# Kernel optimization log

Hardware: AMD Instinct MI355X
Metric: run time of the kernel (lower is better)

Reference implementation:

```python
import jax, jax.numpy as jnp
import numpy as np
from jax import lax

BATCH, SEQ, NMEAS, HID, STATIC, TEMB = 8, 2048, 37, 256, 8, 32
NL, DIN, NST, RANK, K, NLAB = 4, 512, 16, 16, 4, 2  # DIN=expand*HID, RANK=ceil(HID/16)


def rmsnorm(x, w, eps=1e-5):
    return x * lax.rsqrt(jnp.mean(x * x, -1, keepdims=True) + eps) * w


def causal_depthwise_conv(x, w, b):
    # x: [B,L,D], w: [D,K], b: [D]
    L = x.shape[1]
    xpad = jnp.pad(x, ((0, 0), (K - 1, 0), (0, 0)))
    y = sum(w[:, k] * xpad[:, k:k + L, :] for k in range(K))
    return y + b


def selective_scan(u, dt, Bm, Cm, A, Dv):
    # u, dt: [B,L,D]; Bm, Cm: [B,L,N]; A: [D,N]; Dv: [D]
    def step(h, inp):
        dt_t, B_t, C_t, u_t = inp  # [B,D],[B,N],[B,N],[B,D]
        dA = jnp.exp(dt_t[..., None] * A)                      # [B,D,N]
        h = dA * h + dt_t[..., None] * B_t[:, None, :] * u_t[..., None]
        y = jnp.einsum('bdn,bn->bd', h, C_t)
        return h, y

    h0 = jnp.zeros((u.shape[0], DIN, NST), u.dtype)
    xs = (dt.transpose(1, 0, 2), Bm.transpose(1, 0, 2), Cm.transpose(1, 0, 2), u.transpose(1, 0, 2))
    _, ys = lax.scan(step, h0, xs)
    return ys.transpose(1, 0, 2) + u * Dv


def mamba_block(h, nw, ipW, cW, cb, xpW, dpW, dpb, Alog, Dv, opW):
    x = rmsnorm(h, nw)
    proj = x @ ipW.T                     # [B,L,2*DIN]
    xi, z = proj[..., :DIN], proj[..., DIN:]
    xc = jax.nn.silu(causal_depthwise_conv(xi, cW, cb))
    xdbc = xc @ xpW.T                    # [B,L,RANK+2N]
    dt = jax.nn.softplus(xdbc[..., :RANK] @ dpW.T + dpb)
    Bm = xdbc[..., RANK:RANK + NST]
    Cm = xdbc[..., RANK + NST:]
    A = -jnp.exp(Alog)
    y = selective_scan(xc, dt, Bm, Cm, A, Dv)
    y = y * jax.nn.silu(z)
    return h + y @ opW.T


def _forward(time_series_data, static_data, time_array, ts_W, ts_b, t2v_w, t2v_b,
             time_W, time_b, static_W, static_b, ln_g, ln_b, norm_w, in_proj_W,
             conv_W, conv_b, x_proj_W, dt_proj_W, dt_proj_b, A_log, D_skip,
             out_proj_W, normf_w, dense_W, dense_b, head_W, head_b):
    # embeddings: measurement projection + time2vec + static broadcast, then LayerNorm
    x = jnp.einsum('bmt,hm->bth', time_series_data, ts_W) + ts_b    # [B,T,H]
    tv = time_array[..., None] * t2v_w + t2v_b                       # [B,T,TEMB]
    tv = jnp.concatenate([tv[..., :1], jnp.sin(tv[..., 1:])], -1)    # time2vec
    x = x + tv @ time_W.T + time_b
    x = x + (static_data @ static_W.T + static_b)[:, None, :]
    mu = jnp.mean(x, -1, keepdims=True)
    var = jnp.var(x, -1, keepdims=True)
    h = (x - mu) * lax.rsqrt(var + 1e-12) * ln_g + ln_b
    for i in range(NL):
        h = mamba_block(h, norm_w[i], in_proj_W[i], conv_W[i], conv_b[i],
                        x_proj_W[i], dt_proj_W[i], dt_proj_b[i], A_log[i],
                        D_skip[i], out_proj_W[i])
    h = rmsnorm(h, normf_w)
    pooled = jnp.mean(h, 1)                                          # [B,H]
    z = jax.nn.relu(pooled @ dense_W.T + dense_b)
    return z @ head_W.T + head_b                                     # [B,NLAB]


def setup_inputs() -> dict:
    key = jax.random.key(0)
    ks = iter(jax.random.split(key, 48))
    rn = lambda *s: jax.random.normal(next(ks), s, jnp.float32)
    sc = 0.02
    d = {}
    d['time_series_data'] = rn(BATCH, NMEAS, SEQ)
    d['static_data'] = rn(BATCH, STATIC)
    d['time_array'] = jax.random.uniform(next(ks), (BATCH, SEQ), jnp.float32) * 100.0
    d['ts_W'] = rn(HID, NMEAS) * sc; d['ts_b'] = jnp.zeros(HID)
    d['t2v_w'] = rn(TEMB) * sc; d['t2v_b'] = rn(TEMB) * sc
    d['time_W'] = rn(HID, TEMB) * sc; d['time_b'] = jnp.zeros(HID)
    d['static_W'] = rn(HID, STATIC) * sc; d['static_b'] = jnp.zeros(HID)
    d['ln_g'] = jnp.ones(HID); d['ln_b'] = jnp.zeros(HID)
    d['norm_w'] = jnp.ones((NL, HID))
    d['in_proj_W'] = rn(NL, 2 * DIN, HID) * sc
    d['conv_W'] = rn(NL, DIN, K) * sc; d['conv_b'] = jnp.zeros((NL, DIN))
    d['x_proj_W'] = rn(NL, RANK + 2 * NST, DIN) * sc
    d['dt_proj_W'] = rn(NL, DIN, RANK) * sc
    d['dt_proj_b'] = jnp.full((NL, DIN), -4.6) + rn(NL, DIN) * 0.1
    d['A_log'] = jnp.tile(jnp.log(jnp.arange(1, NST + 1, dtype=jnp.float32)), (NL, DIN, 1))
    d['D_skip'] = jnp.ones((NL, DIN))
    d['out_proj_W'] = rn(NL, HID, DIN) * sc
    d['normf_w'] = jnp.ones(HID)
    d['dense_W'] = rn(HID, HID) * sc; d['dense_b'] = jnp.zeros(HID)
    d['head_W'] = rn(NLAB, HID) * sc; d['head_b'] = jnp.zeros(NLAB)
    return d


def reference(time_series_data, static_data, time_array, ts_W, ts_b, t2v_w, t2v_b,
              time_W, time_b, static_W, static_b, ln_g, ln_b, norm_w, in_proj_W,
              conv_W, conv_b, x_proj_W, dt_proj_W, dt_proj_b, A_log, D_skip,
              out_proj_W, normf_w, dense_W, dense_b, head_W, head_b):
    return _forward(time_series_data, static_data, time_array, ts_W, ts_b, t2v_w,
                    t2v_b, time_W, time_b, static_W, static_b, ln_g, ln_b, norm_w,
                    in_proj_W, conv_W, conv_b, x_proj_W, dt_proj_W, dt_proj_b,
                    A_log, D_skip, out_proj_W, normf_w, dense_W, dense_b, head_W, head_b)
```

## Files before the change

### kernel.cpp

```cpp
#include <hip/hip_runtime.h>
#include <math.h>

#define B_ 8
#define T_ 2048
#define HID_ 256
#define DIN_ 512
#define NST_ 16
#define RANK_ 16
#define NL_ 4
#define NC_ 128
#define TC_ 16

typedef unsigned short u16;
typedef unsigned int u32;
typedef __attribute__((ext_vector_type(8))) short bf16x8;
typedef __attribute__((ext_vector_type(4))) float f32x4;

__device__ __forceinline__ float exp2_i(float x) {
  float r; asm("v_exp_f32 %0, %1" : "=v"(r) : "v"(x)); return r;
}
__device__ __forceinline__ float log2_i(float x) {
  float r; asm("v_log_f32 %0, %1" : "=v"(r) : "v"(x)); return r;
}
__device__ __forceinline__ float rcp_i(float x) {
  float r; asm("v_rcp_f32 %0, %1" : "=v"(r) : "v"(x)); return r;
}
#define LOG2E 1.44269504f
#define LN2   0.69314718f

__device__ __forceinline__ float silu_f(float x) {
  return x * rcp_i(1.f + exp2_i(-LOG2E * x));
}
__device__ __forceinline__ float softplus_f(float x) {
  return (x > 20.f) ? x : LN2 * log2_i(1.f + exp2_i(LOG2E * x));
}

__device__ __forceinline__ u16 f2b(float f) {
  union { float f; unsigned u; } v; v.f = f;
  unsigned r = (v.u + 0x7FFFu + ((v.u >> 16) & 1u)) >> 16;
  return (u16)r;
}
__device__ __forceinline__ float b2f(u16 b) {
  union { unsigned u; float f; } v; v.u = ((unsigned)b) << 16;
  return v.f;
}

__device__ __forceinline__ void async16(const void* g, const void* l) {
  __builtin_amdgcn_global_load_lds(
      (const __attribute__((address_space(1))) unsigned int*)g,
      (__attribute__((address_space(3))) unsigned int*)l, 16, 0, 0);
}

__global__ __launch_bounds__(256) void f2b_k(const float* __restrict__ s, u16* __restrict__ d, int n)
{
  int i = (blockIdx.x * 256 + threadIdx.x) * 4;
  if (i + 3 < n) {
    float4 v = *(const float4*)(s + i);
    d[i + 0] = f2b(v.x); d[i + 1] = f2b(v.y); d[i + 2] = f2b(v.z); d[i + 3] = f2b(v.w);
  } else {
    for (int k = i; k < n; k++) d[k] = f2b(s[k]);
  }
}

__global__ __launch_bounds__(256) void a2t_k(const float* __restrict__ Alog, float* __restrict__ a2t)
{
  int idx = blockIdx.x * 256 + threadIdx.x;
  int l = idx >> 13, nd = idx & 8191;
  int n = nd >> 9, d = nd & 511;
  float al = Alog[(size_t)l * 8192 + d * 16 + n];
  a2t[(size_t)l * 8192 + n * 512 + d] = -exp2_i(al * LOG2E) * LOG2E;
}

__global__ __launch_bounds__(512) void wmerge_k(
    const float* __restrict__ dpW,
    const float* __restrict__ xpW,
    u16* __restrict__ wcomb)
{
  int n = blockIdx.x, l = blockIdx.y, k = threadIdx.x;
  const float* xp = xpW + (size_t)l * 48 * 512;
  float acc;
  if (n < 512) {
    const float* dp = dpW + ((size_t)l * 512 + n) * 16;
    acc = 0.f;
    #pragma unroll
    for (int r = 0; r < 16; r++) acc += dp[r] * xp[r * 512 + k];
  } else if (n < 544) {
    acc = xp[(size_t)(16 + n - 512) * 512 + k];
  } else {
    acc = 0.f;
  }
  wcomb[((size_t)l * 640 + n) * 512 + k] = f2b(acc);
}

__global__ __launch_bounds__(256) void embed_ln_k(
    const float* __restrict__ tsd, const float* __restrict__ stat, const float* __restrict__ ta,
    const float* __restrict__ tsW, const float* __restrict__ tsb,
    const float* __restrict__ t2vw, const float* __restrict__ t2vb,
    const float* __restrict__ timeW, const float* __restrict__ timeb,
    const float* __restrict__ statW, const float* __restrict__ statb,
    const float* __restrict__ lng, const float* __restrict__ lnb,
    const float* __restrict__ nw0,
    float* __restrict__ hout, u16* __restrict__ xnb)
{
  __shared__ float xts[37 * 32];
  __shared__ float tvs[32 * 32];
  __shared__ float outs[32 * 257];
  __shared__ float smu[32], srs[32], srs2[32];
  int blk = blockIdx.x;
  int b = blk >> 6, t0 = (blk & 63) * 32;
  int j = threadIdx.x;

  float wts[37], wtv[32], wst[8];
  #pragma unroll
  for (int m = 0; m < 37; m++) wts[m] = tsW[j * 37 + m];
  #pragma unroll
  for (int e = 0; e < 32; e++) wtv[e] = timeW[j * 32 + e];
  #pragma unroll
  for (int s = 0; s < 8; s++) wst[s] = statW[j * 8 + s];
  float biasj = tsb[j] + timeb[j] + statb[j];
  float lngj = lng[j], lnbj = lnb[j];
  float nw0j = nw0[j];
  float stq[8];
  #pragma unroll
  for (int s = 0; s < 8; s++) stq[s] = stat[b * 8 + s];

  for (int idx = j; idx < 37 * 32; idx += 256) {
    int m = idx >> 5, tt = idx & 31;
    xts[idx] = tsd[((size_t)b * 37 + m) * T_ + t0 + tt];
  }
  {
    int rr = j >> 5, ee = j & 31;
    #pragma unroll
    for (int rp = 0; rp < 4; rp++) {
      int r = rp * 8 + rr;
      float tav = ta[b * T_ + t0 + r];
      float tv = tav * t2vw[ee] + t2vb[ee];
      tvs[r * 32 + ee] = (ee == 0) ? tv : sinf(tv);
    }
  }
  __syncthreads();

  for (int r = 0; r < 32; r++) {
    float acc = biasj;
    #pragma unroll
    for (int m = 0; m < 37; m++) acc += xts[m * 32 + r] * wts[m];
    #pragma unroll
    for (int e = 0; e < 32; e++) acc += tvs[r * 32 + e] * wtv[e];
    #pragma unroll
    for (int s = 0; s < 8; s++) acc += stq[s] * wst[s];
    outs[r * 257 + j] = acc;
  }
  __syncthreads();
  {
    int r = j >> 3, q = j & 7;
    const float* po = &outs[r * 257 + q * 32];
    float s = 0.f, ss = 0.f;
    #pragma unroll
    for (int i = 0; i < 32; i++) { float v = po[i]; s += v; ss += v * v; }
    s += __shfl_down(s, 1, 64); ss += __shfl_down(ss, 1, 64);
    s += __shfl_down(s, 2, 64); ss += __shfl_down(ss, 2, 64);
    s += __shfl_down(s, 4, 64); ss += __shfl_down(ss, 4, 64);
    if (q == 0) {
      float mu = s * (1.f / 256.f);
      smu[r] = mu;
      srs[r] = rsqrtf(ss * (1.f / 256.f) - mu * mu + 1e-12f);
    }
  }
  __syncthreads();
  for (int r = 0; r < 32; r++) {
    float v = outs[r * 257 + j];
    float hv = (v - smu[r]) * srs[r] * lngj + lnbj;
    hout[((size_t)(b * T_ + t0 + r)) * HID_ + j] = hv;
    outs[r * 257 + j] = hv;
  }
  __syncthreads();
  {
    int r = j >> 3, q = j & 7;
    const float* po = &outs[r * 257 + q * 32];
    float ss = 0.f;
    #pragma unroll
    for (int i = 0; i < 32; i++) { float v = po[i]; ss += v * v; }
    ss += __shfl_down(ss, 1, 64);
    ss += __shfl_down(ss, 2, 64);
    ss += __shfl_down(ss, 4, 64);
    if (q == 0) srs2[r] = rsqrtf(ss * (1.f / 256.f) + 1e-5f);
  }
  __syncthreads();
  for (int r = 0; r < 32; r++) {
    xnb[((size_t)(b * T_ + t0 + r)) * HID_ + j] = f2b(outs[r * 257 + j] * srs2[r] * nw0j);
  }
}

template <int MODE>
__global__ __launch_bounds__(256) void mgemm_k(
    const u16* __restrict__ A, int lda,
    const u16* __restrict__ W, int ldw,
    void* __restrict__ Cv, int ldc,
    int K,
    const float* __restrict__ bias,
    void* __restrict__ Cv2)
{
  __shared__ u16 smem[128 * 136];
  u16* sA = smem;
  u16* sB = smem + 128 * 64;
  const int tid = threadIdx.x;
  const int bm = blockIdx.x * 128, bn = blockIdx.y * 128;
  const int w = tid >> 6, l = tid & 63;
  const int wm = (w & 1) * 64, wn = (w >> 1) * 64;
  const int lr = l & 15, lh = l >> 4;

  f32x4 acc[4][4] = {};

  const int srow = tid >> 3;
  const int schunk = tid & 7;

  for (int k0 = 0; k0 < K; k0 += 64) {
    #pragma unroll
    for (int c = 0; c < 4; c++) {
      int row = c * 32 + srow;
      int g = schunk ^ (row & 7);
      async16(A + (size_t)(bm + row) * lda + k0 + g * 8, &sA[c * 2048 + w * 512]);
      async16(W + (size_t)(bn + row) * ldw + k0 + g * 8, &sB[c * 2048 + w * 512]);
    }
    __syncthreads();
    #pragma unroll
    for (int kk = 0; kk < 2; kk++) {
      bf16x8 af[4], bfr[4];
      #pragma unroll
      for (int i = 0; i < 4; i++) {
        int ra = wm + i * 16 + lr;
        int rb = wn + i * 16 + lr;
        int e = kk * 4 + lh;
        af[i]  = *(const bf16x8*)&sA[ra * 64 + ((e ^ (ra & 7)) * 8)];
        bfr[i] = *(const bf16x8*)&sB[rb * 64 + ((e ^ (rb & 7)) * 8)];
      }
      #pragma unroll
      for (int i = 0; i < 4; i++)
        #pragma unroll
        for (int j = 0; j < 4; j++)
          acc[i][j] = __builtin_amdgcn_mfma_f32_16x16x32_bf16(af[i], bfr[j], acc[i][j], 0, 0, 0);
    }
    __syncthreads();
  }

  if (MODE == 6 && bn >= 512) {
    #pragma unroll
    for (int i = 0; i < 4; i++) {
      int m = bm + wm + i * 16 + lh * 4;
      #pragma unroll
      for (int j = 0; j < 4; j++) {
        int n = bn + wn + j * 16 + lr;
        if (n < 544) {
          #pragma unroll
          for (int r = 0; r < 4; r++)
            ((float*)Cv2)[(size_t)(m + r) * 32 + (n - 512)] = acc[i][j][r];
        }
      }
    }
  } else {
    u16* eps = smem;
    float bv[4];
    if (MODE == 6) {
      #pragma unroll
      for (int j = 0; j < 4; j++) bv[j] = bias[bn + wn + j * 16 + lr];
    }
    #pragma unroll
    for (int i = 0; i < 4; i++) {
      int rr = wm + i * 16 + lh * 4;
      #pragma unroll
      for (int j = 0; j < 4; j++) {
        int cc = wn + j * 16 + lr;
        #pragma unroll
        for (int r = 0; r < 4; r++) {
          float v = acc[i][j][r];
          if (MODE == 6) v = softplus_f(v + bv[j]);
          eps[(rr + r) * 136 + cc] = f2b(v);
        }
      }
    }
    __syncthreads();
    u16* dbase; int c0;
    if (MODE == 4 && bn >= 512) { dbase = (u16*)Cv2; c0 = bn - 512; }
    else                        { dbase = (u16*)Cv;  c0 = bn; }
    #pragma unroll
    for (int q = 0; q < 8; q++) {
      int flat = q * 256 + tid;
      int row = flat >> 4, cv = flat & 15;
      *(uint4*)&dbase[(size_t)(bm + row) * 512 + c0 + cv * 8] =
          *(const uint4*)&eps[row * 136 + cv * 8];
    }
  }
}

__global__ __launch_bounds__(256) void mgemm7_k(
    const u16* __restrict__ A,
    const u16* __restrict__ W,
    float* __restrict__ h,
    const float* __restrict__ nw,
    u16* __restrict__ xnb)
{
  __shared__ u16 smem[20480];
  __shared__ float rns[2][64];
  __shared__ float snw[256];
  u16* sA = smem;
  u16* sB = smem + 4096;
  const int tid = threadIdx.x;
  const int bm = blockIdx.x * 64;
  const int w = tid >> 6, l = tid & 63;
  const int wm = (w & 1) * 32, wn = (w >> 1) * 128;
  const int lr = l & 15, lh = l >> 4;

  if (tid < 256) snw[tid] = nw[tid];

  f32x4 acc[2][8] = {};

  const int srow = tid >> 3;
  const int schunk = tid & 7;

  for (int k0 = 0; k0 < 512; k0 += 64) {
    #pragma unroll
    for (int c = 0; c < 2; c++) {
      int row = c * 32 + srow;
      int g = schunk ^ (row & 7);
      async16(A + (size_t)(bm + row) * 512 + k0 + g * 8, &sA[c * 2048 + w * 512]);
    }
    #pragma unroll
    for (int c = 0; c < 8; c++) {
      int row = c * 32 + srow;
      int g = schunk ^ (row & 7);
      async16(W + (size_t)row * 512 + k0 + g * 8, &sB[c * 2048 + w * 512]);
    }
    __syncthreads();
    #pragma unroll
    for (int kk = 0; kk < 2; kk++) {
      int e = kk * 4 + lh;
      bf16x8 af[2], bfr[8];
      #pragma unroll
      for (int i = 0; i < 2; i++) {
        int ra = wm + i * 16 + lr;
        af[i] = *(const bf16x8*)&sA[ra * 64 + ((e ^ (ra & 7)) * 8)];
      }
      #pragma unroll
      for (int j = 0; j < 8; j++) {
        int rb = wn + j * 16 + lr;
        bfr[j] = *(const bf16x8*)&sB[rb * 64 + ((e ^ (rb & 7)) * 8)];
      }
      #pragma unroll
      for (int i = 0; i < 2; i++)
        #pragma unroll
        for (int j = 0; j < 8; j++)
          acc[i][j] = __builtin_amdgcn_mfma_f32_16x16x32_bf16(af[i], bfr[j], acc[i][j], 0, 0, 0);
    }
    __syncthreads();
  }

  #pragma unroll
  for (int i = 0; i < 2; i++) {
    int m = bm + wm + i * 16 + lh * 4;
    #pragma unroll
    for (int j = 0; j < 8; j++) {
      int n = wn + j * 16 + lr;
      float* cp = h + (size_t)m * 256 + n;
      #pragma unroll
      for (int r = 0; r < 4; r++) {
        float hv = acc[i][j][r] + cp[(size_t)r * 256];
        cp[(size_t)r * 256] = hv;
        acc[i][j][r] = hv;
      }
    }
  }
  #pragma unroll
  for (int i = 0; i < 2; i++) {
    #pragma unroll
    for (int r = 0; r < 4; r++) {
      float p = 0.f;
      #pragma unroll
      for (int j = 0; j < 8; j++) { float v = acc[i][j][r]; p += v * v; }
      p += __shfl_xor(p, 1, 64);
      p += __shfl_xor(p, 2, 64);
      p += __shfl_xor(p, 4, 64);
      p += __shfl_xor(p, 8, 64);
      if (lr == 0) rns[w >> 1][wm + i * 16 + lh * 4 + r] = p;
    }
  }
  __syncthreads();
  u16* eps = smem;
  #pragma unroll
  for (int i = 0; i < 2; i++) {
    #pragma unroll
    for (int r = 0; r < 4; r++) {
      int rl = wm + i * 16 + lh * 4 + r;
      float rs = rsqrtf((rns[0][rl] + rns[1][rl]) * (1.f / 256.f) + 1e-5f);
      #pragma unroll
      for (int j = 0; j < 8; j++) {
        int n = wn + j * 16 + lr;
        eps[rl * 264 + n] = f2b(acc[i][j][r] * rs * snw[n]);
      }
    }
  }
  __syncthreads();
  #pragma unroll
  for (int q = 0; q < 8; q++) {
    int flat = q * 256 + tid;
    int row = flat >> 5, cv = flat & 31;
    *(uint4*)&xnb[(size_t)(bm + row) * 256 + cv * 8] =
        *(const uint4*)&eps[row * 264 + cv * 8];
  }
}

__global__ __launch_bounds__(256) void conv_silu_k(
    const u16* __restrict__ xib,
    const float* __restrict__ cw,
    const float* __restrict__ cb,
    u16* __restrict__ xcb)
{
  int idx = blockIdx.x * 256 + threadIdx.x;
  int row = idx >> 6;
  int t = row & (T_ - 1);
  int d0 = (idx & 63) << 3;

  float acc[8];
  *(float4*)&acc[0] = *(const float4*)&cb[d0];
  *(float4*)&acc[4] = *(const float4*)&cb[d0 + 4];
  float wreg[8][4];
  #pragma unroll
  for (int j = 0; j < 8; j++)
    *(float4*)&wreg[j][0] = *(const float4*)&cw[(d0 + j) * 4];

  #pragma unroll
  for (int k = 0; k < 4; k++) {
    int tt = t + k - 3;
    if (tt >= 0) {
      bf16x8 v = *(const bf16x8*)&xib[(size_t)(row + k - 3) * 512 + d0];
      #pragma unroll
      for (int j = 0; j < 8; j++) acc[j] += wreg[j][k] * b2f((u16)v[j]);
    }
  }
  u16 o[8];
  #pragma unroll
  for (int j = 0; j < 8; j++) o[j] = f2b(silu_f(acc[j]));
  *(bf16x8*)&xcb[(size_t)row * 512 + d0] = *(const bf16x8*)o;
}

__global__ __launch_bounds__(512) void scan_passA_k(
    const u16* __restrict__ xcb,
    const u16* __restrict__ dtb,
    const float* __restrict__ xdbc,
    const float* __restrict__ a2t,
    u16* __restrict__ chH, float* __restrict__ dts)
{
  __shared__ float sDBC[TC_ * 32];
  int c = blockIdx.x, b = blockIdx.y, d = threadIdx.x;
  size_t base_row = (size_t)(b * T_ + c * TC_);

  if (d < 128) async16(xdbc + base_row * 32 + d * 4, &sDBC[(d >> 6) * 256]);

  float a2[16], hl[16];
  #pragma unroll
  for (int n = 0; n < 16; n++) { a2[n] = a2t[n * 512 + d]; hl[n] = 0.f; }
  float dtsum = 0.f;
  const u16* up = xcb + base_row * 512 + d;
  const u16* tp = dtb + base_row * 512 + d;
  u16 pu = up[0], pt = tp[0];
  __syncthreads();

  #pragma unroll 1
  for (int s = 0; s < TC_; s++) {
    float u   = b2f(pu);
    float dtv = b2f(pt);
    int sn = (s + 1 < TC_) ? s + 1 : s;
    pu = up[(size_t)sn * 512];
    pt = tp[(size_t)sn * 512];
    dtsum += dtv;
    float du = dtv * u;
    const float* rowp = &sDBC[s * 32];
    #pragma unroll
    for (int g = 0; g < 4; g++) {
      float4 b4 = *(const float4*)&rowp[g * 4];
      int i = g * 4;
      float dA0 = exp2_i(dtv * a2[i + 0]); hl[i + 0] = dA0 * hl[i + 0] + du * b4.x;
      float dA1 = exp2_i(dtv * a2[i + 1]); hl[i + 1] = dA1 * hl[i + 1] + du * b4.y;
      float dA2 = exp2_i(dtv * a2[i + 2]); hl[i + 2] = dA2 * hl[i + 2] + du * b4.z;
      float dA3 = exp2_i(dtv * a2[i + 3]); hl[i + 3] = dA3 * hl[i + 3] + du * b4.w;
    }
  }
  u16 oh[16];
  #pragma unroll
  for (int n = 0; n < 16; n++) oh[n] = f2b(hl[n]);
  size_t o = ((size_t)((b * NC_ + c) * DIN_ + d)) * 16;
  *(uint4*)&chH[o]     = *(const uint4*)&oh[0];
  *(uint4*)&chH[o + 8] = *(const uint4*)&oh[8];
  dts[(size_t)(b * NC_ + c) * DIN_ + d] = dtsum;
}

__global__ __launch_bounds__(256) void scan_mid_k(
    const u32* __restrict__ chH32, const float* __restrict__ dts,
    const float* __restrict__ a2t, u32* __restrict__ hin32)
{
  int idx = blockIdx.x * 256 + threadIdx.x;
  int b = idx >> 12, dk = idx & 4095;
  int d = dk >> 3, k = dk & 7;
  float a20 = a2t[(2 * k) * 512 + d];
  float a21 = a2t[(2 * k + 1) * 512 + d];
  float h0 = 0.f, h1 = 0.f;
  #pragma unroll 8
  for (int c = 0; c < NC_; c++) {
    size_t o = ((size_t)(b * NC_ + c)) * 4096 + dk;
    u32 hh = chH32[o];
    float dsv = dts[(size_t)(b * NC_ + c) * 512 + d];
    hin32[o] = ((u32)f2b(h1) << 16) | (u32)f2b(h0);
    float ap0 = exp2_i(a20 * dsv);
    float ap1 = exp2_i(a21 * dsv);
    h0 = ap0 * h0 + b2f((u16)(hh & 0xffff));
    h1 = ap1 * h1 + b2f((u16)(hh >> 16));
  }
}

__global__ __launch_bounds__(512) void scan_passC_k(
    const u16* __restrict__ xcb,
    const u16* __restrict__ dtb,
    const u16* __restrict__ zb,
    const float* __restrict__ xdbc,
    const float* __restrict__ a2t,
    const u16* __restrict__ hin,
    const float* __restrict__ Dv,
    u16* __restrict__ yzb)
{
  __shared__ float sDBC[TC_ * 32];
  int c = blockIdx.x, b = blockIdx.y, d = threadIdx.x;
  size_t base_row = (size_t)(b * T_ + c * TC_);

  if (d < 128) async16(xdbc + base_row * 32 + d * 4, &sDBC[(d >> 6) * 256]);

  float a2[16], hs[16];
  {
    size_t ho = ((size_t)((b * NC_ + c) * DIN_ + d)) * 16;
    uint4 h0 = *(const uint4*)&hin[ho];
    uint4 h1 = *(const uint4*)&hin[ho + 8];
    const u32* hw = (const u32*)&h0;
    #pragma unroll
    for (int j = 0; j < 4; j++) {
      hs[2 * j]     = b2f((u16)(hw[j] & 0xffff));
      hs[2 * j + 1] = b2f((u16)(hw[j] >> 16));
    }
    const u32* hw1 = (const u32*)&h1;
    #pragma unroll
    for (int j = 0; j < 4; j++) {
      hs[8 + 2 * j]     = b2f((u16)(hw1[j] & 0xffff));
      hs[8 + 2 * j + 1] = b2f((u16)(hw1[j] >> 16));
    }
  }
  #pragma unroll
  for (int n = 0; n < 16; n++) a2[n] = a2t[n * 512 + d];
  float dv = Dv[d];
  const u16* up = xcb + base_row * 512 + d;
  const u16* tp = dtb + base_row * 512 + d;
  const u16* zp = zb + base_row * 512 + d;
  u16 pu = up[0], pt = tp[0], zz = zp[0];
  __syncthreads();

  #pragma unroll 1
  for (int s = 0; s < TC_; s++) {
    float u   = b2f(pu);
    float dtv = b2f(pt);
    float z   = b2f(zz);
    int sn = (s + 1 < TC_) ? s + 1 : s;
    pu = up[(size_t)sn * 512];
    pt = tp[(size_t)sn * 512];
    zz = zp[(size_t)sn * 512];
    float du = dtv * u;
    float y = 0.f;
    const float* rowp = &sDBC[s * 32];
    #pragma unroll
    for (int g = 0; g < 4; g++) {
      float4 b4 = *(const float4*)&rowp[g * 4];
      float4 c4 = *(const float4*)&rowp[16 + g * 4];
      int i = g * 4;
      float dA0 = exp2_i(dtv * a2[i + 0]); hs[i + 0] = dA0 * hs[i + 0] + du * b4.x; y += hs[i + 0] * c4.x;
      float dA1 = exp2_i(dtv * a2[i + 1]); hs[i + 1] = dA1 * hs[i + 1] + du * b4.y; y += hs[i + 1] * c4.y;
      float dA2 = exp2_i(dtv * a2[i + 2]); hs[i + 2] = dA2 * hs[i + 2] + du * b4.z; y += hs[i + 2] * c4.z;
      float dA3 = exp2_i(dtv * a2[i + 3]); hs[i + 3] = dA3 * hs[i + 3] + du * b4.w; y += hs[i + 3] * c4.w;
    }
    y += u * dv;
    yzb[(base_row + s) * DIN_ + d] = f2b(y * silu_f(z));
  }
}

__global__ __launch_bounds__(256) void pool_partial_k(const u16* __restrict__ xn, float* __restrict__ poolP)
{
  int b = blockIdx.x, tc = blockIdx.y, j = threadIdx.x;
  float s = 0.f;
  int t0 = tc * 256;
  #pragma unroll 4
  for (int tt = 0; tt < 256; tt++)
    s += b2f(xn[((size_t)(b * T_ + t0 + tt)) * HID_ + j]);
  poolP[(b * 8 + tc) * HID_ + j] = s;
}

__global__ __launch_bounds__(256) void head_k(
    const float* __restrict__ poolP,
    const float* __restrict__ denW, const float* __restrict__ denb,
    const float* __restrict__ hdW, const float* __restrict__ hdb,
    float* __restrict__ out)
{
  int b = blockIdx.x, j = threadIdx.x;
  float p = 0.f;
  #pragma unroll
  for (int tc = 0; tc < 8; tc++) p += poolP[(b * 8 + tc) * HID_ + j];
  p *= (1.f / 2048.f);
  __shared__ float pl[256], zs[256];
  pl[j] = p;
  __syncthreads();
  float acc = denb[j];
  #pragma unroll 8
  for (int k = 0; k < 256; k++) acc += pl[k] * denW[j * 256 + k];
  zs[j] = fmaxf(acc, 0.f);
  __syncthreads();
  if (j < 2) {
    float o = hdb[j];
    for (int k = 0; k < 256; k++) o += zs[k] * hdW[j * 256 + k];
    out[b * 2 + j] = o;
  }
}

extern "C" void kernel_launch(void* const* d_in, const int* in_sizes, int n_in,
                              void* d_out, int out_size, void* d_ws, size_t ws_size,
                              hipStream_t stream)
{
  const float* tsd   = (const float*)d_in[0];
  const float* stat  = (const float*)d_in[1];
  const float* ta    = (const float*)d_in[2];
  const float* tsW   = (const float*)d_in[3];
  const float* tsb   = (const float*)d_in[4];
  const float* t2vw  = (const float*)d_in[5];
  const float* t2vb  = (const float*)d_in[6];
  const float* timeW = (const float*)d_in[7];
  const float* timeb = (const float*)d_in[8];
  const float* statW = (const float*)d_in[9];
  const float* statb = (const float*)d_in[10];
  const float* lng   = (const float*)d_in[11];
  const float* lnb   = (const float*)d_in[12];
  const float* normw = (const float*)d_in[13];
  const float* ipW   = (const float*)d_in[14];
  const float* convW = (const float*)d_in[15];
  const float* convb = (const float*)d_in[16];
  const float* xpW   = (const float*)d_in[17];
  const float* dpW   = (const float*)d_in[18];
  const float* dpb   = (const float*)d_in[19];
  const float* Alog  = (const float*)d_in[20];
  const float* Dsk   = (const float*)d_in[21];
  const float* opW   = (const float*)d_in[22];
  const float* normf = (const float*)d_in[23];
  const float* denW  = (const float*)d_in[24];
  const float* denb  = (const float*)d_in[25];
  const float* hdW   = (const float*)d_in[26];
  const float* hdb   = (const float*)d_in[27];
  float* out = (float*)d_out;

  float* ws = (float*)d_ws;
  float* h    = ws;  ws += (size_t)B_ * T_ * HID_;
  float* xdbc = ws;  ws += (size_t)B_ * T_ * 32;
  float* poolP= ws;  ws += (size_t)B_ * 8 * HID_;
  float* a2t  = ws;  ws += (size_t)NL_ * NST_ * DIN_;
  float* dts  = ws;  ws += (size_t)B_ * NC_ * DIN_;
  u16* chH    = (u16*)ws;  ws += (size_t)B_ * NC_ * DIN_ * NST_ / 2;
  u16* hin    = (u16*)ws;  ws += (size_t)B_ * NC_ * DIN_ * NST_ / 2;
  u16* dtb    = (u16*)ws;  ws += (size_t)B_ * T_ * DIN_ / 2;
  u16* xi_b   = (u16*)ws;  ws += (size_t)B_ * T_ * DIN_ / 2;
  u16* z_b    = (u16*)ws;  ws += (size_t)B_ * T_ * DIN_ / 2;
  u16* xn_b   = (u16*)ws;  ws += (size_t)B_ * T_ * HID_ / 2;
  u16* xcb    = (u16*)ws;  ws += (size_t)B_ * T_ * DIN_ / 2;
  u16* yz_b   = (u16*)ws;  ws += (size_t)B_ * T_ * DIN_ / 2;
  u16* wipb   = (u16*)ws;  ws += (size_t)NL_ * 1024 * HID_ / 2;
  u16* wopb   = (u16*)ws;  ws += (size_t)NL_ * HID_ * DIN_ / 2;
  u16* wcomb  = (u16*)ws;  ws += (size_t)NL_ * 640 * DIN_ / 2;

  const int ROWS = B_ * T_;

  {
    int nip = NL_ * 1024 * HID_;
    int nop = NL_ * HID_ * DIN_;
    f2b_k<<<nip / 1024, 256, 0, stream>>>(ipW, wipb, nip);
    f2b_k<<<nop / 1024, 256, 0, stream>>>(opW, wopb, nop);
    a2t_k<<<NL_ * NST_ * DIN_ / 256, 256, 0, stream>>>(Alog, a2t);
    wmerge_k<<<dim3(640, NL_), 512, 0, stream>>>(dpW, xpW, wcomb);
  }

  embed_ln_k<<<512, 256, 0, stream>>>(tsd, stat, ta, tsW, tsb, t2vw, t2vb,
                                      timeW, timeb, statW, statb, lng, lnb,
                                      normw, h, xn_b);

  for (int i = 0; i < NL_; i++) {
    const u16* wipbi = wipb + (size_t)i * 1024 * HID_;
    const u16* wopbi = wopb + (size_t)i * HID_ * DIN_;
    const u16* wcombi = wcomb + (size_t)i * 640 * DIN_;
    const float* dpbi = dpb + (size_t)i * DIN_;
    const float* a2ti = a2t + (size_t)i * NST_ * DIN_;
    const float* nw_next = (i < NL_ - 1) ? (normw + (i + 1) * HID_) : normf;

    mgemm_k<4><<<dim3(ROWS / 128, 8), 256, 0, stream>>>(
        xn_b, HID_, wipbi, HID_, xi_b, 512, HID_, nullptr, z_b);
    conv_silu_k<<<ROWS * 64 / 256, 256, 0, stream>>>(xi_b, convW + i * DIN_ * 4, convb + i * DIN_, xcb);
    mgemm_k<6><<<dim3(ROWS / 128, 5), 256, 0, stream>>>(
        xcb, DIN_, wcombi, DIN_, dtb, 512, DIN_, dpbi, xdbc);
    scan_passA_k<<<dim3(NC_, B_), DIN_, 0, stream>>>(xcb, dtb, xdbc, a2ti, chH, dts);
    scan_mid_k<<<B_ * DIN_ * 8 / 256, 256, 0, stream>>>((const u32*)chH, dts, a2ti, (u32*)hin);
    scan_passC_k<<<dim3(NC_, B_), DIN_, 0, stream>>>(xcb, dtb, z_b, xdbc, a2ti, hin,
                                                     Dsk + i * DIN_, yz_b);
    mgemm7_k<<<ROWS / 64, 256, 0, stream>>>(yz_b, wopbi, h, nw_next, xn_b);
  }

  pool_partial_k<<<dim3(B_, 8), 256, 0, stream>>>(xn_b, poolP);
  head_k<<<B_, 256, 0, stream>>>(poolP, denW, denb, hdW, hdb, out);
}
```

Before: 700.4 us.

## Fuse pooling into final out-proj GEMM, merge prep kernels, register-reuse conv

On the last layer, the output-projection GEMM now reduces the normalized rows straight into per-batch pooled sums with atomics, so it no longer writes h, the bf16 xn buffer or runs a separate pooling kernel. The weight-conversion and A-transform kernels are merged into one launch. The causal conv now computes four timesteps per thread, reusing the loaded input rows from registers. Atomic accumulation changes the floating-point summation order, and a memset is added.

```diff
diff --git a/kernel.cpp b/kernel.cpp
--- a/kernel.cpp
+++ b/kernel.cpp
@@ -51,24 +51,29 @@
       (__attribute__((address_space(3))) unsigned int*)l, 16, 0, 0);
 }
 
-__global__ __launch_bounds__(256) void f2b_k(const float* __restrict__ s, u16* __restrict__ d, int n)
-{
-  int i = (blockIdx.x * 256 + threadIdx.x) * 4;
-  if (i + 3 < n) {
-    float4 v = *(const float4*)(s + i);
-    d[i + 0] = f2b(v.x); d[i + 1] = f2b(v.y); d[i + 2] = f2b(v.z); d[i + 3] = f2b(v.w);
+__global__ __launch_bounds__(256) void prep_k(
+    const float* __restrict__ ipW, u16* __restrict__ wipb,
+    const float* __restrict__ opW, u16* __restrict__ wopb,
+    const float* __restrict__ Alog, float* __restrict__ a2t)
+{
+  int blk = blockIdx.x;
+  if (blk < 1024) {
+    int i = (blk * 256 + threadIdx.x) * 4;
+    float4 v = *(const float4*)(ipW + i);
+    wipb[i + 0] = f2b(v.x); wipb[i + 1] = f2b(v.y);
+    wipb[i + 2] = f2b(v.z); wipb[i + 3] = f2b(v.w);
+  } else if (blk < 1536) {
+    int i = ((blk - 1024) * 256 + threadIdx.x) * 4;
+    float4 v = *(const float4*)(opW + i);
+    wopb[i + 0] = f2b(v.x); wopb[i + 1] = f2b(v.y);
+    wopb[i + 2] = f2b(v.z); wopb[i + 3] = f2b(v.w);
   } else {
-    for (int k = i; k < n; k++) d[k] = f2b(s[k]);
-  }
-}
-
-__global__ __launch_bounds__(256) void a2t_k(const float* __restrict__ Alog, float* __restrict__ a2t)
-{
-  int idx = blockIdx.x * 256 + threadIdx.x;
-  int l = idx >> 13, nd = idx & 8191;
-  int n = nd >> 9, d = nd & 511;
-  float al = Alog[(size_t)l * 8192 + d * 16 + n];
-  a2t[(size_t)l * 8192 + n * 512 + d] = -exp2_i(al * LOG2E) * LOG2E;
+    int idx = (blk - 1536) * 256 + threadIdx.x;
+    int l = idx >> 13, nd = idx & 8191;
+    int n = nd >> 9, d = nd & 511;
+    float al = Alog[(size_t)l * 8192 + d * 16 + n];
+    a2t[(size_t)l * 8192 + n * 512 + d] = -exp2_i(al * LOG2E) * LOG2E;
+  }
 }
 
 __global__ __launch_bounds__(512) void wmerge_k(
@@ -292,12 +297,14 @@
   }
 }
 
+template <int LAST>
 __global__ __launch_bounds__(256) void mgemm7_k(
     const u16* __restrict__ A,
     const u16* __restrict__ W,
     float* __restrict__ h,
     const float* __restrict__ nw,
-    u16* __restrict__ xnb)
+    u16* __restrict__ xnb,
+    float* __restrict__ poolP)
 {
   __shared__ u16 smem[20480];
   __shared__ float rns[2][64];
@@ -364,7 +371,7 @@
       #pragma unroll
       for (int r = 0; r < 4; r++) {
         float hv = acc[i][j][r] + cp[(size_t)r * 256];
-        cp[(size_t)r * 256] = hv;
+        if (!LAST) cp[(size_t)r * 256] = hv;
         acc[i][j][r] = hv;
       }
     }
@@ -384,27 +391,46 @@
     }
   }
   __syncthreads();
-  u16* eps = smem;
-  #pragma unroll
-  for (int i = 0; i < 2; i++) {
-    #pragma unroll
-    for (int r = 0; r < 4; r++) {
-      int rl = wm + i * 16 + lh * 4 + r;
-      float rs = rsqrtf((rns[0][rl] + rns[1][rl]) * (1.f / 256.f) + 1e-5f);
-      #pragma unroll
-      for (int j = 0; j < 8; j++) {
-        int n = wn + j * 16 + lr;
-        eps[rl * 264 + n] = f2b(acc[i][j][r] * rs * snw[n]);
+  if (LAST) {
+    int b = bm >> 11;
+    #pragma unroll
+    for (int j = 0; j < 8; j++) {
+      int n = wn + j * 16 + lr;
+      float colp = 0.f;
+      #pragma unroll
+      for (int i = 0; i < 2; i++) {
+        #pragma unroll
+        for (int r = 0; r < 4; r++) {
+          int rl = wm + i * 16 + lh * 4 + r;
+          float rs = rsqrtf((rns[0][rl] + rns[1][rl]) * (1.f / 256.f) + 1e-5f);
+          colp += acc[i][j][r] * rs;
+        }
       }
-    }
-  }
-  __syncthreads();
-  #pragma unroll
-  for (int q = 0; q < 8; q++) {
-    int flat = q * 256 + tid;
-    int row = flat >> 5, cv = flat & 31;
-    *(uint4*)&xnb[(size_t)(bm + row) * 256 + cv * 8] =
-        *(const uint4*)&eps[row * 264 + cv * 8];
+      atomicAdd(&poolP[b * 256 + n], colp * snw[n]);
+    }
+  } else {
+    u16* eps = smem;
+    #pragma unroll
+    for (int i = 0; i < 2; i++) {
+      #pragma unroll
+      for (int r = 0; r < 4; r++) {
+        int rl = wm + i * 16 + lh * 4 + r;
+        float rs = rsqrtf((rns[0][rl] + rns[1][rl]) * (1.f / 256.f) + 1e-5f);
+        #pragma unroll
+        for (int j = 0; j < 8; j++) {
+          int n = wn + j * 16 + lr;
+          eps[rl * 264 + n] = f2b(acc[i][j][r] * rs * snw[n]);
+        }
+      }
+    }
+    __syncthreads();
+    #pragma unroll
+    for (int q = 0; q < 8; q++) {
+      int flat = q * 256 + tid;
+      int row = flat >> 5, cv = flat & 31;
+      *(uint4*)&xnb[(size_t)(bm + row) * 256 + cv * 8] =
+          *(const uint4*)&eps[row * 264 + cv * 8];
+    }
   }
 }
 
@@ -415,31 +441,45 @@
     u16* __restrict__ xcb)
 {
   int idx = blockIdx.x * 256 + threadIdx.x;
-  int row = idx >> 6;
-  int t = row & (T_ - 1);
+  int row0 = (idx >> 6) * 4;
+  int t0 = row0 & (T_ - 1);
   int d0 = (idx & 63) << 3;
 
-  float acc[8];
-  *(float4*)&acc[0] = *(const float4*)&cb[d0];
-  *(float4*)&acc[4] = *(const float4*)&cb[d0 + 4];
   float wreg[8][4];
   #pragma unroll
   for (int j = 0; j < 8; j++)
     *(float4*)&wreg[j][0] = *(const float4*)&cw[(d0 + j) * 4];
-
-  #pragma unroll
-  for (int k = 0; k < 4; k++) {
-    int tt = t + k - 3;
+  float4 cbl = *(const float4*)&cb[d0];
+  float4 cbh = *(const float4*)&cb[d0 + 4];
+
+  bf16x8 xv[7];
+  #pragma unroll
+  for (int r = 0; r < 7; r++) {
+    int tt = t0 - 3 + r;
     if (tt >= 0) {
-      bf16x8 v = *(const bf16x8*)&xib[(size_t)(row + k - 3) * 512 + d0];
+      xv[r] = *(const bf16x8*)&xib[(size_t)(row0 - 3 + r) * 512 + d0];
+    } else {
+      #pragma unroll
+      for (int j = 0; j < 8; j++) xv[r][j] = 0;
+    }
+  }
+
+  #pragma unroll
+  for (int o = 0; o < 4; o++) {
+    float acc[8];
+    acc[0] = cbl.x; acc[1] = cbl.y; acc[2] = cbl.z; acc[3] = cbl.w;
+    acc[4] = cbh.x; acc[5] = cbh.y; acc[6] = cbh.z; acc[7] = cbh.w;
+    #pragma unroll
+    for (int k = 0; k < 4; k++) {
+      bf16x8 v = xv[o + k];
       #pragma unroll
       for (int j = 0; j < 8; j++) acc[j] += wreg[j][k] * b2f((u16)v[j]);
     }
-  }
-  u16 o[8];
-  #pragma unroll
-  for (int j = 0; j < 8; j++) o[j] = f2b(silu_f(acc[j]));
-  *(bf16x8*)&xcb[(size_t)row * 512 + d0] = *(const bf16x8*)o;
+    u16 ot[8];
+    #pragma unroll
+    for (int j = 0; j < 8; j++) ot[j] = f2b(silu_f(acc[j]));
+    *(bf16x8*)&xcb[(size_t)(row0 + o) * 512 + d0] = *(const bf16x8*)ot;
+  }
 }
 
 __global__ __launch_bounds__(512) void scan_passA_k(
@@ -586,17 +626,6 @@
   }
 }
 
-__global__ __launch_bounds__(256) void pool_partial_k(const u16* __restrict__ xn, float* __restrict__ poolP)
-{
-  int b = blockIdx.x, tc = blockIdx.y, j = threadIdx.x;
-  float s = 0.f;
-  int t0 = tc * 256;
-  #pragma unroll 4
-  for (int tt = 0; tt < 256; tt++)
-    s += b2f(xn[((size_t)(b * T_ + t0 + tt)) * HID_ + j]);
-  poolP[(b * 8 + tc) * HID_ + j] = s;
-}
-
 __global__ __launch_bounds__(256) void head_k(
     const float* __restrict__ poolP,
     const float* __restrict__ denW, const float* __restrict__ denb,
@@ -604,10 +633,7 @@
     float* __restrict__ out)
 {
   int b = blockIdx.x, j = threadIdx.x;
-  float p = 0.f;
-  #pragma unroll
-  for (int tc = 0; tc < 8; tc++) p += poolP[(b * 8 + tc) * HID_ + j];
-  p *= (1.f / 2048.f);
+  float p = poolP[b * 256 + j] * (1.f / 2048.f);
   __shared__ float pl[256], zs[256];
   pl[j] = p;
   __syncthreads();
@@ -660,7 +686,7 @@
   float* ws = (float*)d_ws;
   float* h    = ws;  ws += (size_t)B_ * T_ * HID_;
   float* xdbc = ws;  ws += (size_t)B_ * T_ * 32;
-  float* poolP= ws;  ws += (size_t)B_ * 8 * HID_;
+  float* poolP= ws;  ws += (size_t)B_ * HID_;
   float* a2t  = ws;  ws += (size_t)NL_ * NST_ * DIN_;
   float* dts  = ws;  ws += (size_t)B_ * NC_ * DIN_;
   u16* chH    = (u16*)ws;  ws += (size_t)B_ * NC_ * DIN_ * NST_ / 2;
@@ -677,14 +703,9 @@
 
   const int ROWS = B_ * T_;
 
-  {
-    int nip = NL_ * 1024 * HID_;
-    int nop = NL_ * HID_ * DIN_;
-    f2b_k<<<nip / 1024, 256, 0, stream>>>(ipW, wipb, nip);
-    f2b_k<<<nop / 1024, 256, 0, stream>>>(opW, wopb, nop);
-    a2t_k<<<NL_ * NST_ * DIN_ / 256, 256, 0, stream>>>(Alog, a2t);
-    wmerge_k<<<dim3(640, NL_), 512, 0, stream>>>(dpW, xpW, wcomb);
-  }
+  hipMemsetAsync(poolP, 0, (size_t)B_ * HID_ * sizeof(float), stream);
+  prep_k<<<1664, 256, 0, stream>>>(ipW, wipb, opW, wopb, Alog, a2t);
+  wmerge_k<<<dim3(640, NL_), 512, 0, stream>>>(dpW, xpW, wcomb);
 
   embed_ln_k<<<512, 256, 0, stream>>>(tsd, stat, ta, tsW, tsb, t2vw, t2vb,
                                       timeW, timeb, statW, statb, lng, lnb,
@@ -700,16 +721,19 @@
 
     mgemm_k<4><<<dim3(ROWS / 128, 8), 256, 0, stream>>>(
         xn_b, HID_, wipbi, HID_, xi_b, 512, HID_, nullptr, z_b);
-    conv_silu_k<<<ROWS * 64 / 256, 256, 0, stream>>>(xi_b, convW + i * DIN_ * 4, convb + i * DIN_, xcb);
+    conv_silu_k<<<ROWS * 16 / 256, 256, 0, stream>>>(xi_b, convW + i * DIN_ * 4, convb + i * DIN_, xcb);
     mgemm_k<6><<<dim3(ROWS / 128, 5), 256, 0, stream>>>(
         xcb, DIN_, wcombi, DIN_, dtb, 512, DIN_, dpbi, xdbc);
     scan_passA_k<<<dim3(NC_, B_), DIN_, 0, stream>>>(xcb, dtb, xdbc, a2ti, chH, dts);
     scan_mid_k<<<B_ * DIN_ * 8 / 256, 256, 0, stream>>>((const u32*)chH, dts, a2ti, (u32*)hin);
     scan_passC_k<<<dim3(NC_, B_), DIN_, 0, stream>>>(xcb, dtb, z_b, xdbc, a2ti, hin,
                                                      Dsk + i * DIN_, yz_b);
-    mgemm7_k<<<ROWS / 64, 256, 0, stream>>>(yz_b, wopbi, h, nw_next, xn_b);
-  }
-
-  pool_partial_k<<<dim3(B_, 8), 256, 0, stream>>>(xn_b, poolP);
+    if (i < NL_ - 1) {
+      mgemm7_k<0><<<ROWS / 64, 256, 0, stream>>>(yz_b, wopbi, h, nw_next, xn_b, poolP);
+    } else {
+      mgemm7_k<1><<<ROWS / 64, 256, 0, stream>>>(yz_b, wopbi, h, nw_next, xn_b, poolP);
+    }
+  }
+
   head_k<<<B_, 256, 0, stream>>>(poolP, denW, denb, hdW, hdb, out);
 }
```

Result: faster. 612.3 us (-12.6%).
